# Kernel optimization log

Measured on AMD Instinct MI355X. Metric: run time of the kernel, lower is better.

Reference implementation:

```python
import jax, jax.numpy as jnp
import numpy as np
import math

B, N_NODES, N_EDGES = 2, 20000, 320000
IN_DIM, MODEL_DIM, NUM_HEADS = 128, 128, 8
HEAD_DIM = MODEL_DIM // NUM_HEADS
EPS = 1e-5


def setup_inputs() -> dict:
    key = jax.random.key(0)
    ks = jax.random.split(key, 12)
    s = 0.02
    x = jax.random.normal(ks[0], (B, N_NODES, IN_DIM), dtype=jnp.float32)
    edge_index = jax.random.randint(ks[1], (2, N_EDGES), 0, N_NODES, dtype=jnp.int32)
    return {
        "x": x,
        "proj_w": jax.random.normal(ks[2], (IN_DIM, MODEL_DIM), jnp.float32) * s,
        "wq_w": jax.random.normal(ks[3], (MODEL_DIM, MODEL_DIM), jnp.float32) * s,
        "wq_b": jax.random.normal(ks[4], (MODEL_DIM,), jnp.float32) * s,
        "wk_w": jax.random.normal(ks[5], (MODEL_DIM, MODEL_DIM), jnp.float32) * s,
        "wk_b": jax.random.normal(ks[6], (MODEL_DIM,), jnp.float32) * s,
        "wv_w": jax.random.normal(ks[7], (MODEL_DIM, MODEL_DIM), jnp.float32) * s,
        "wv_b": jax.random.normal(ks[8], (MODEL_DIM,), jnp.float32) * s,
        "ln_g": jnp.ones((MODEL_DIM,), jnp.float32),
        "ln_b": jnp.zeros((MODEL_DIM,), jnp.float32),
        "edge_index": edge_index,
    }


def reference(x, proj_w, wq_w, wq_b, wk_w, wk_b, wv_w, wv_b, ln_g, ln_b, edge_index):
    src, dst = edge_index[0], edge_index[1]
    scale = 1.0 / math.sqrt(HEAD_DIM)

    h = x @ proj_w                      # [B, N, D]  (dropout = identity in eval)
    lifted = h[:, src, :]               # [B, E, D] edge gather
    Q = lifted @ wq_w + wq_b
    K = lifted @ wk_w + wk_b
    V = lifted @ wv_w + wv_b

    alpha = jnp.sum(Q * K, axis=-1) * scale  # [B, E]

    def seg_softmax(a):  # a: [E]
        m = jax.ops.segment_max(a, dst, num_segments=N_NODES)
        m = jnp.where(jnp.isfinite(m), m, 0.0)
        e = jnp.exp(a - m[dst])
        s = jax.ops.segment_sum(e, dst, num_segments=N_NODES)
        return e / s[dst]

    attn = jax.vmap(seg_softmax)(alpha)           # [B, E]
    weighted_V = V * attn[..., None]              # [B, E, D]

    seg_sum = lambda t: jax.ops.segment_sum(t, dst, num_segments=N_NODES)
    agg = jax.vmap(seg_sum)(weighted_V)           # [B, N, D]

    counts = jax.ops.segment_sum(jnp.ones((N_EDGES,), jnp.float32), dst,
                                 num_segments=N_NODES)
    skip = jax.vmap(seg_sum)(lifted) / jnp.maximum(counts, 1.0)[None, :, None]

    out = agg + skip
    mu = jnp.mean(out, axis=-1, keepdims=True)
    var = jnp.var(out, axis=-1, keepdims=True)
    return (out - mu) * jax.lax.rsqrt(var + EPS) * ln_g + ln_b
```

## Files before the change

kernel.cpp:

```cpp
#include <hip/hip_runtime.h>
#include <hip/hip_bf16.h>

#define NNODES 20000
#define NEDGES 320000
#define BATCH  2
#define D      128
#define EPSF   1e-5f
#define QTM    64
#define XS_LD  136
#define MAXDEG 64
#define NROWS  (BATCH * NNODES)

typedef __attribute__((ext_vector_type(8))) short bf16x8;
typedef __attribute__((ext_vector_type(4))) float f32x4;

static __device__ __forceinline__ unsigned short f2bf(float f) {
    __hip_bfloat16 h = __float2bfloat16(f);
    return *reinterpret_cast<unsigned short*>(&h);
}
static __device__ __forceinline__ float bfu(unsigned short u) {
    union { unsigned int i; float f; } cv;
    cv.i = ((unsigned int)u) << 16;
    return cv.f;
}

__global__ __launch_bounds__(256) void prep_kernel(
    const float* __restrict__ Wp, const float* __restrict__ Wq,
    const float* __restrict__ Wk, const float* __restrict__ Wv,
    unsigned short* __restrict__ WF,
    int* __restrict__ cursor)
{
    int bid = blockIdx.x;
    if (bid < 32) {
        int sg = bid * 256 + threadIdx.x;
        int mat = sg >> 11, rem = sg & 2047;
        int f = rem >> 6, l = rem & 63;
        int nt = f >> 2, ks = f & 3;
        int c = l & 15, g = l >> 4;
        const float* W = (mat == 0) ? Wp : (mat == 1) ? Wq : (mat == 2) ? Wk : Wv;
        int n = nt * 16 + c;
        #pragma unroll
        for (int i = 0; i < 8; ++i) {
            int k = ks * 32 + g * 8 + i;
            WF[(size_t)sg * 8 + i] = f2bf(W[k * 128 + n]);
        }
    } else {
        int idx = (bid - 32) * 256 + threadIdx.x;
        if (idx < NNODES) cursor[idx] = 0;
    }
}

__global__ __launch_bounds__(256) void scatter_pad_kernel(
    const int* __restrict__ src, const int* __restrict__ dst,
    int* __restrict__ cursor,
    int* __restrict__ srcs_pad)
{
    int e = blockIdx.x * 256 + threadIdx.x;
    if (e >= NEDGES) return;
    int d = dst[e], s = src[e];
    int slot = atomicAdd(&cursor[d], 1);
    if (slot < MAXDEG) srcs_pad[d * MAXDEG + slot] = s;
}

#define DECL_STAGE_MACROS                                               \
    bf16x8 wreg[8];
#define LOAD_W_REGS(MAT_OFF)                                            \
    _Pragma("unroll")                                                   \
    for (int q = 0; q < 8; ++q)                                         \
        wreg[q] = *(const bf16x8*)(WF + (MAT_OFF) + (q * 256 + t) * 8);
#define WRITE_W_LDS()                                                   \
    _Pragma("unroll")                                                   \
    for (int q = 0; q < 8; ++q)                                         \
        *(bf16x8*)&Wbuf[(q * 256 + t) * 8] = wreg[q];


__global__ __launch_bounds__(256) void hv_kernel(
    const float* __restrict__ x,
    const unsigned short* __restrict__ WF,
    const float* __restrict__ Bv,
    unsigned short* __restrict__ hhv)
{
    __shared__ unsigned short Wbuf[16384];
    __shared__ unsigned short Hs[4][16][XS_LD];
    const int t = threadIdx.x;
    const long row0 = (long)blockIdx.x * QTM;
    const int w = t >> 6, l = t & 63;
    const int g = l >> 4, c = l & 15;
    const int rw = w * 16;
    DECL_STAGE_MACROS

    LOAD_W_REGS(0)

    bf16x8 ax[4];
    {
        const float* xr = x + (row0 + rw + c) * D;
        #pragma unroll
        for (int ks = 0; ks < 4; ++ks) {
            float4 u0 = *(const float4*)(xr + ks * 32 + g * 8);
            float4 u1 = *(const float4*)(xr + ks * 32 + g * 8 + 4);
            bf16x8 f;
            f[0] = (short)f2bf(u0.x); f[1] = (short)f2bf(u0.y);
            f[2] = (short)f2bf(u0.z); f[3] = (short)f2bf(u0.w);
            f[4] = (short)f2bf(u1.x); f[5] = (short)f2bf(u1.y);
            f[6] = (short)f2bf(u1.z); f[7] = (short)f2bf(u1.w);
            ax[ks] = f;
        }
    }

    WRITE_W_LDS();
    __syncthreads();
    LOAD_W_REGS(49152)

    f32x4 hacc[8];
    #pragma unroll
    for (int nt = 0; nt < 8; ++nt) hacc[nt] = f32x4{0.f, 0.f, 0.f, 0.f};
    #pragma unroll
    for (int nt = 0; nt < 8; ++nt)
        #pragma unroll
        for (int ks = 0; ks < 4; ++ks) {
            bf16x8 b = *(const bf16x8*)&Wbuf[((nt * 4 + ks) * 64 + l) * 8];
            hacc[nt] = __builtin_amdgcn_mfma_f32_16x16x32_bf16(ax[ks], b, hacc[nt], 0, 0, 0);
        }
    #pragma unroll
    for (int nt = 0; nt < 8; ++nt)
        #pragma unroll
        for (int i = 0; i < 4; ++i)
            Hs[w][4 * g + i][nt * 16 + c] = f2bf(hacc[nt][i]);

    #pragma unroll
    for (int q = 0; q < 4; ++q) {
        int ch = q * 64 + l;
        int r = ch >> 4, off = (ch & 15) << 3;
        *(bf16x8*)(hhv + (row0 + rw + r) * 256 + off) = *(const bf16x8*)&Hs[w][r][off];
    }
    bf16x8 ah[4];
    #pragma unroll
    for (int ks = 0; ks < 4; ++ks)
        ah[ks] = *(const bf16x8*)&Hs[w][c][ks * 32 + g * 8];

    __syncthreads();
    WRITE_W_LDS();
    __syncthreads();

    #pragma unroll
    for (int nt = 0; nt < 8; ++nt) {
        f32x4 vacc = f32x4{0.f, 0.f, 0.f, 0.f};
        #pragma unroll
        for (int ks = 0; ks < 4; ++ks) {
            bf16x8 b = *(const bf16x8*)&Wbuf[((nt * 4 + ks) * 64 + l) * 8];
            vacc = __builtin_amdgcn_mfma_f32_16x16x32_bf16(ah[ks], b, vacc, 0, 0, 0);
        }
        float bv = Bv[nt * 16 + c];
        #pragma unroll
        for (int i = 0; i < 4; ++i)
            Hs[w][4 * g + i][nt * 16 + c] = f2bf(vacc[i] + bv);
    }
    #pragma unroll
    for (int q = 0; q < 4; ++q) {
        int ch = q * 64 + l;
        int r = ch >> 4, off = (ch & 15) << 3;
        *(bf16x8*)(hhv + (row0 + rw + r) * 256 + 128 + off) = *(const bf16x8*)&Hs[w][r][off];
    }
}

__global__ __launch_bounds__(256) void alpha_kernel(
    const unsigned short* __restrict__ hhv,
    const unsigned short* __restrict__ WF,
    const float* __restrict__ Bq, const float* __restrict__ Bk,
    float* __restrict__ a_out)
{
    __shared__ unsigned short Wbuf[16384];
    const int t = threadIdx.x;
    const long row0 = (long)blockIdx.x * QTM;
    const int w = t >> 6, l = t & 63;
    const int g = l >> 4, c = l & 15;
    const int rw = w * 16;
    DECL_STAGE_MACROS

    LOAD_W_REGS(16384)

    bf16x8 ah[4];
    {
        const unsigned short* hr = hhv + (row0 + rw + c) * 256;
        #pragma unroll
        for (int ks = 0; ks < 4; ++ks)
            ah[ks] = *(const bf16x8*)(hr + ks * 32 + g * 8);
    }

    WRITE_W_LDS();
    __syncthreads();
    LOAD_W_REGS(32768)

    f32x4 qacc[8];
    #pragma unroll
    for (int nt = 0; nt < 8; ++nt) qacc[nt] = f32x4{0.f, 0.f, 0.f, 0.f};
    #pragma unroll
    for (int nt = 0; nt < 8; ++nt)
        #pragma unroll
        for (int ks = 0; ks < 4; ++ks) {
            bf16x8 b = *(const bf16x8*)&Wbuf[((nt * 4 + ks) * 64 + l) * 8];
            qacc[nt] = __builtin_amdgcn_mfma_f32_16x16x32_bf16(ah[ks], b, qacc[nt], 0, 0, 0);
        }
    __syncthreads();
    WRITE_W_LDS();
    __syncthreads();

    float p[4] = {0.f, 0.f, 0.f, 0.f};
    #pragma unroll
    for (int nt = 0; nt < 8; ++nt) {
        f32x4 kacc = f32x4{0.f, 0.f, 0.f, 0.f};
        #pragma unroll
        for (int ks = 0; ks < 4; ++ks) {
            bf16x8 b = *(const bf16x8*)&Wbuf[((nt * 4 + ks) * 64 + l) * 8];
            kacc = __builtin_amdgcn_mfma_f32_16x16x32_bf16(ah[ks], b, kacc, 0, 0, 0);
        }
        float bq = Bq[nt * 16 + c];
        float bk = Bk[nt * 16 + c];
        #pragma unroll
        for (int i = 0; i < 4; ++i)
            p[i] += (qacc[nt][i] + bq) * (kacc[i] + bk);
    }
    #pragma unroll
    for (int off = 1; off < 16; off <<= 1)
        #pragma unroll
        for (int i = 0; i < 4; ++i) p[i] += __shfl_xor(p[i], off, 64);
    if (c == 0)
        #pragma unroll
        for (int i = 0; i < 4; ++i)
            a_out[row0 + rw + 4 * g + i] = p[i] * 0.25f;
}

__global__ __launch_bounds__(256) void agg_kernel(
    const unsigned short* __restrict__ hhv,
    const float* __restrict__ a,
    const int* __restrict__ deg_arr,
    const int* __restrict__ srcs_pad,
    const float* __restrict__ ln_g, const float* __restrict__ ln_b,
    float* __restrict__ out)
{
    const int t = threadIdx.x;
    const int w = t >> 6, l = t & 63;
    const int flat = blockIdx.x * 4 + w;
    const int n = flat % NNODES;
    const int b = flat / NNODES;
    const int bN = b * NNODES;
    const int deg = min(deg_arr[n], MAXDEG);
    const bool valid = l < deg;

    int   sr_l = valid ? srcs_pad[n * MAXDEG + l] : 0;
    float av_l = valid ? a[bN + sr_l] : -1e30f;

    float m = av_l;
    #pragma unroll
    for (int off = 32; off >= 1; off >>= 1) m = fmaxf(m, __shfl_xor(m, off, 64));
    float e_l = valid ? __expf(av_l - m) : 0.f;
    float s = e_l;
    #pragma unroll
    for (int off = 32; off >= 1; off >>= 1) s += __shfl_xor(s, off, 64);
    const float inv_s = (deg > 0) ? 1.f / s : 0.f;
    const float inv_d = 1.f / (float)max(deg, 1);
    const float w_l = e_l * inv_s;

    const int eh   = l >> 5;
    const int half = (l >> 4) & 1;
    const int cq   = l & 15;
    float acc[8] = {0,0,0,0,0,0,0,0};
    const long rowBase = (long)bN * 256 + half * 128 + (cq << 3);

    #define PREP(JJ, OF, MU)  {                                         \
        int sel = ((JJ) << 1) + eh;                                     \
        bool ev = sel < deg;                                            \
        int sc = ev ? sel : 0;                                          \
        int srj = __shfl(sr_l, sc, 64);                                 \
        float wj = __shfl(w_l, sc, 64);                                 \
        MU = half ? (ev ? wj : 0.f) : (ev ? 1.f : 0.f);                 \
        OF = rowBase + (long)srj * 256;  }

    const int iters = (deg + 1) >> 1;
    for (int j0 = 0; j0 < iters; j0 += 4) {
        long oa, ob, oc, od; float ma, mb, mc, md;
        PREP(j0,     oa, ma)
        PREP(j0 + 1, ob, mb)
        PREP(j0 + 2, oc, mc)
        PREP(j0 + 3, od, md)
        bf16x8 da = *(const bf16x8*)(hhv + oa);
        bf16x8 db = *(const bf16x8*)(hhv + ob);
        bf16x8 dc = *(const bf16x8*)(hhv + oc);
        bf16x8 dd = *(const bf16x8*)(hhv + od);
        #pragma unroll
        for (int i = 0; i < 8; ++i) acc[i] += ma * bfu((unsigned short)da[i]);
        #pragma unroll
        for (int i = 0; i < 8; ++i) acc[i] += mb * bfu((unsigned short)db[i]);
        #pragma unroll
        for (int i = 0; i < 8; ++i) acc[i] += mc * bfu((unsigned short)dc[i]);
        #pragma unroll
        for (int i = 0; i < 8; ++i) acc[i] += md * bfu((unsigned short)dd[i]);
    }
    #undef PREP

    float accv[8], sk[8];
    #pragma unroll
    for (int i = 0; i < 8; ++i) {
        float other = __shfl_xor(acc[i], 16, 64);
        accv[i] = half ? acc[i] : other;
        sk[i]   = half ? other  : acc[i];
    }
    #pragma unroll
    for (int i = 0; i < 8; ++i) {
        accv[i] += __shfl_xor(accv[i], 32, 64);
        sk[i]   += __shfl_xor(sk[i],   32, 64);
    }
    float v[8];
    float sum = 0.f, sq = 0.f;
    #pragma unroll
    for (int i = 0; i < 8; ++i) {
        v[i] = accv[i] + sk[i] * inv_d;
        sum += v[i];
        sq  += v[i] * v[i];
    }
    #pragma unroll
    for (int off = 8; off >= 1; off >>= 1) {
        sum += __shfl_xor(sum, off, 64);
        sq  += __shfl_xor(sq,  off, 64);
    }
    float mu   = sum * (1.f / 128.f);
    float var  = sq * (1.f / 128.f) - mu * mu;
    float rstd = rsqrtf(var + EPSF);
    if (l < 16) {
        float4 g0 = *(const float4*)(ln_g + (cq << 3));
        float4 g1 = *(const float4*)(ln_g + (cq << 3) + 4);
        float4 b0 = *(const float4*)(ln_b + (cq << 3));
        float4 b1 = *(const float4*)(ln_b + (cq << 3) + 4);
        float4 o0, o1;
        o0.x = (v[0] - mu) * rstd * g0.x + b0.x;
        o0.y = (v[1] - mu) * rstd * g0.y + b0.y;
        o0.z = (v[2] - mu) * rstd * g0.z + b0.z;
        o0.w = (v[3] - mu) * rstd * g0.w + b0.w;
        o1.x = (v[4] - mu) * rstd * g1.x + b1.x;
        o1.y = (v[5] - mu) * rstd * g1.y + b1.y;
        o1.z = (v[6] - mu) * rstd * g1.z + b1.z;
        o1.w = (v[7] - mu) * rstd * g1.w + b1.w;
        float* op = out + (long)flat * D + (cq << 3);
        *(float4*)op = o0;
        *(float4*)(op + 4) = o1;
    }
}


extern "C" void kernel_launch(void* const* d_in, const int* in_sizes, int n_in,
                              void* d_out, int out_size, void* d_ws, size_t ws_size,
                              hipStream_t stream)
{
    const float* x    = (const float*)d_in[0];
    const float* Wp   = (const float*)d_in[1];
    const float* Wq   = (const float*)d_in[2];
    const float* Bq   = (const float*)d_in[3];
    const float* Wk   = (const float*)d_in[4];
    const float* Bk   = (const float*)d_in[5];
    const float* Wv   = (const float*)d_in[6];
    const float* Bv   = (const float*)d_in[7];
    const float* ln_g = (const float*)d_in[8];
    const float* ln_b = (const float*)d_in[9];
    const int*   ei   = (const int*)d_in[10];
    const int* esrc = ei;
    const int* edst = ei + NEDGES;
    float* out = (float*)d_out;

    char* p = (char*)d_ws;
    auto alloc = [&](size_t bytes) -> char* {
        char* r = p;
        p += (bytes + 255) & ~(size_t)255;
        return r;
    };
    unsigned short* hhv = (unsigned short*)alloc((size_t)NROWS * 256 * 2);
    float* a        = (float*)alloc((size_t)NROWS * 4);
    int* cursor     = (int*)alloc((size_t)NNODES * 4);
    int* srcs_pad   = (int*)alloc((size_t)NNODES * MAXDEG * 4);
    unsigned short* WF = (unsigned short*)alloc((size_t)4 * 128 * 128 * 2);

    prep_kernel<<<111, 256, 0, stream>>>(Wp, Wq, Wk, Wv, WF, cursor);
    scatter_pad_kernel<<<(NEDGES + 255) / 256, 256, 0, stream>>>(esrc, edst, cursor, srcs_pad);
    hv_kernel<<<NROWS / QTM, 256, 0, stream>>>(x, WF, Bv, hhv);
    alpha_kernel<<<NROWS / QTM, 256, 0, stream>>>(hhv, WF, Bq, Bk, a);
    agg_kernel<<<NROWS / 4, 256, 0, stream>>>(hhv, a, cursor, srcs_pad, ln_g, ln_b, out);
}
```

Before: 164.3 us.

## Apply V projection after aggregation instead of per node before gather

Because attention weights sum to one, the V projection and its bias commute with the weighted segment sum. The code therefore aggregates bf16 h rows, both attention-weighted and mean-weighted, and applies Wv in a new final kernel that also does the residual add and LayerNorm. The gather now reads 128-wide h rows instead of 256-wide h|V rows, which halves gather bandwidth. In exchange it adds a kernel launch and an intermediate buffer round-trip, and the final kernel uses uncoalesced scalar loads and stores.

```diff
diff --git a/kernel.cpp b/kernel.cpp
--- a/kernel.cpp
+++ b/kernel.cpp
@@ -73,12 +73,10 @@
     for (int q = 0; q < 8; ++q)                                         \
         *(bf16x8*)&Wbuf[(q * 256 + t) * 8] = wreg[q];
 
-
-__global__ __launch_bounds__(256) void hv_kernel(
+__global__ __launch_bounds__(256) void h_kernel(
     const float* __restrict__ x,
     const unsigned short* __restrict__ WF,
-    const float* __restrict__ Bv,
-    unsigned short* __restrict__ hhv)
+    unsigned short* __restrict__ h_out)
 {
     __shared__ unsigned short Wbuf[16384];
     __shared__ unsigned short Hs[4][16][XS_LD];
@@ -109,7 +107,6 @@
 
     WRITE_W_LDS();
     __syncthreads();
-    LOAD_W_REGS(49152)
 
     f32x4 hacc[8];
     #pragma unroll
@@ -126,45 +123,16 @@
         #pragma unroll
         for (int i = 0; i < 4; ++i)
             Hs[w][4 * g + i][nt * 16 + c] = f2bf(hacc[nt][i]);
-
     #pragma unroll
     for (int q = 0; q < 4; ++q) {
         int ch = q * 64 + l;
         int r = ch >> 4, off = (ch & 15) << 3;
-        *(bf16x8*)(hhv + (row0 + rw + r) * 256 + off) = *(const bf16x8*)&Hs[w][r][off];
-    }
-    bf16x8 ah[4];
-    #pragma unroll
-    for (int ks = 0; ks < 4; ++ks)
-        ah[ks] = *(const bf16x8*)&Hs[w][c][ks * 32 + g * 8];
-
-    __syncthreads();
-    WRITE_W_LDS();
-    __syncthreads();
-
-    #pragma unroll
-    for (int nt = 0; nt < 8; ++nt) {
-        f32x4 vacc = f32x4{0.f, 0.f, 0.f, 0.f};
-        #pragma unroll
-        for (int ks = 0; ks < 4; ++ks) {
-            bf16x8 b = *(const bf16x8*)&Wbuf[((nt * 4 + ks) * 64 + l) * 8];
-            vacc = __builtin_amdgcn_mfma_f32_16x16x32_bf16(ah[ks], b, vacc, 0, 0, 0);
-        }
-        float bv = Bv[nt * 16 + c];
-        #pragma unroll
-        for (int i = 0; i < 4; ++i)
-            Hs[w][4 * g + i][nt * 16 + c] = f2bf(vacc[i] + bv);
-    }
-    #pragma unroll
-    for (int q = 0; q < 4; ++q) {
-        int ch = q * 64 + l;
-        int r = ch >> 4, off = (ch & 15) << 3;
-        *(bf16x8*)(hhv + (row0 + rw + r) * 256 + 128 + off) = *(const bf16x8*)&Hs[w][r][off];
+        *(bf16x8*)(h_out + (row0 + rw + r) * D + off) = *(const bf16x8*)&Hs[w][r][off];
     }
 }
 
 __global__ __launch_bounds__(256) void alpha_kernel(
-    const unsigned short* __restrict__ hhv,
+    const unsigned short* __restrict__ h,
     const unsigned short* __restrict__ WF,
     const float* __restrict__ Bq, const float* __restrict__ Bk,
     float* __restrict__ a_out)
@@ -181,7 +149,7 @@
 
     bf16x8 ah[4];
     {
-        const unsigned short* hr = hhv + (row0 + rw + c) * 256;
+        const unsigned short* hr = h + (row0 + rw + c) * D;
         #pragma unroll
         for (int ks = 0; ks < 4; ++ks)
             ah[ks] = *(const bf16x8*)(hr + ks * 32 + g * 8);
@@ -231,12 +199,12 @@
 }
 
 __global__ __launch_bounds__(256) void agg_kernel(
-    const unsigned short* __restrict__ hhv,
+    const unsigned short* __restrict__ h,
     const float* __restrict__ a,
     const int* __restrict__ deg_arr,
     const int* __restrict__ srcs_pad,
-    const float* __restrict__ ln_g, const float* __restrict__ ln_b,
-    float* __restrict__ out)
+    const float* __restrict__ Bv,
+    unsigned short* __restrict__ HwS)
 {
     const int t = threadIdx.x;
     const int w = t >> 6, l = t & 63;
@@ -261,88 +229,138 @@
     const float inv_d = 1.f / (float)max(deg, 1);
     const float w_l = e_l * inv_s;
 
-    const int eh   = l >> 5;
-    const int half = (l >> 4) & 1;
-    const int cq   = l & 15;
-    float acc[8] = {0,0,0,0,0,0,0,0};
-    const long rowBase = (long)bN * 256 + half * 128 + (cq << 3);
-
-    #define PREP(JJ, OF, MU)  {                                         \
-        int sel = ((JJ) << 1) + eh;                                     \
+    const int eh = l >> 4;
+    const int cq = l & 15;
+    float aw[8] = {0,0,0,0,0,0,0,0};
+    float au[8] = {0,0,0,0,0,0,0,0};
+    const long base = ((long)bN << 7) + (cq << 3);
+
+    #define PREP(JJ, OF, WW, UU)  {                                     \
+        int sel = ((JJ) << 2) + eh;                                     \
         bool ev = sel < deg;                                            \
         int sc = ev ? sel : 0;                                          \
         int srj = __shfl(sr_l, sc, 64);                                 \
         float wj = __shfl(w_l, sc, 64);                                 \
-        MU = half ? (ev ? wj : 0.f) : (ev ? 1.f : 0.f);                 \
-        OF = rowBase + (long)srj * 256;  }
-
-    const int iters = (deg + 1) >> 1;
-    for (int j0 = 0; j0 < iters; j0 += 4) {
-        long oa, ob, oc, od; float ma, mb, mc, md;
-        PREP(j0,     oa, ma)
-        PREP(j0 + 1, ob, mb)
-        PREP(j0 + 2, oc, mc)
-        PREP(j0 + 3, od, md)
-        bf16x8 da = *(const bf16x8*)(hhv + oa);
-        bf16x8 db = *(const bf16x8*)(hhv + ob);
-        bf16x8 dc = *(const bf16x8*)(hhv + oc);
-        bf16x8 dd = *(const bf16x8*)(hhv + od);
-        #pragma unroll
-        for (int i = 0; i < 8; ++i) acc[i] += ma * bfu((unsigned short)da[i]);
-        #pragma unroll
-        for (int i = 0; i < 8; ++i) acc[i] += mb * bfu((unsigned short)db[i]);
-        #pragma unroll
-        for (int i = 0; i < 8; ++i) acc[i] += mc * bfu((unsigned short)dc[i]);
-        #pragma unroll
-        for (int i = 0; i < 8; ++i) acc[i] += md * bfu((unsigned short)dd[i]);
+        WW = ev ? wj : 0.f;                                             \
+        UU = ev ? 1.f : 0.f;                                            \
+        OF = base + ((long)srj << 7);  }
+
+    const int iters = (deg + 3) >> 2;
+    for (int j0 = 0; j0 < iters; j0 += 2) {
+        long oa, ob; float wa, ua, wb, ub;
+        PREP(j0,     oa, wa, ua)
+        PREP(j0 + 1, ob, wb, ub)
+        bf16x8 da = *(const bf16x8*)(h + oa);
+        bf16x8 db = *(const bf16x8*)(h + ob);
+        #pragma unroll
+        for (int i = 0; i < 8; ++i) {
+            float fv = bfu((unsigned short)da[i]);
+            aw[i] += wa * fv;
+            au[i] += ua * fv;
+        }
+        #pragma unroll
+        for (int i = 0; i < 8; ++i) {
+            float fv = bfu((unsigned short)db[i]);
+            aw[i] += wb * fv;
+            au[i] += ub * fv;
+        }
     }
     #undef PREP
 
-    float accv[8], sk[8];
     #pragma unroll
     for (int i = 0; i < 8; ++i) {
-        float other = __shfl_xor(acc[i], 16, 64);
-        accv[i] = half ? acc[i] : other;
-        sk[i]   = half ? other  : acc[i];
-    }
-    #pragma unroll
-    for (int i = 0; i < 8; ++i) {
-        accv[i] += __shfl_xor(accv[i], 32, 64);
-        sk[i]   += __shfl_xor(sk[i],   32, 64);
-    }
-    float v[8];
-    float sum = 0.f, sq = 0.f;
-    #pragma unroll
-    for (int i = 0; i < 8; ++i) {
-        v[i] = accv[i] + sk[i] * inv_d;
-        sum += v[i];
-        sq  += v[i] * v[i];
-    }
-    #pragma unroll
-    for (int off = 8; off >= 1; off >>= 1) {
-        sum += __shfl_xor(sum, off, 64);
-        sq  += __shfl_xor(sq,  off, 64);
-    }
-    float mu   = sum * (1.f / 128.f);
-    float var  = sq * (1.f / 128.f) - mu * mu;
-    float rstd = rsqrtf(var + EPSF);
+        aw[i] += __shfl_xor(aw[i], 16, 64);
+        au[i] += __shfl_xor(au[i], 16, 64);
+        aw[i] += __shfl_xor(aw[i], 32, 64);
+        au[i] += __shfl_xor(au[i], 32, 64);
+    }
     if (l < 16) {
-        float4 g0 = *(const float4*)(ln_g + (cq << 3));
-        float4 g1 = *(const float4*)(ln_g + (cq << 3) + 4);
-        float4 b0 = *(const float4*)(ln_b + (cq << 3));
-        float4 b1 = *(const float4*)(ln_b + (cq << 3) + 4);
-        float4 o0, o1;
-        o0.x = (v[0] - mu) * rstd * g0.x + b0.x;
-        o0.y = (v[1] - mu) * rstd * g0.y + b0.y;
-        o0.z = (v[2] - mu) * rstd * g0.z + b0.z;
-        o0.w = (v[3] - mu) * rstd * g0.w + b0.w;
-        o1.x = (v[4] - mu) * rstd * g1.x + b1.x;
-        o1.y = (v[5] - mu) * rstd * g1.y + b1.y;
-        o1.z = (v[6] - mu) * rstd * g1.z + b1.z;
-        o1.w = (v[7] - mu) * rstd * g1.w + b1.w;
-        float* op = out + (long)flat * D + (cq << 3);
-        *(float4*)op = o0;
-        *(float4*)(op + 4) = o1;
+        const float bvm = (deg > 0) ? 1.f : 0.f;
+        bf16x8 w8, s8;
+        #pragma unroll
+        for (int i = 0; i < 8; ++i) {
+            w8[i] = (short)f2bf(aw[i]);
+            s8[i] = (short)f2bf(au[i] * inv_d + bvm * Bv[(cq << 3) + i]);
+        }
+        unsigned short* op = HwS + (long)flat * 256 + (cq << 3);
+        *(bf16x8*)op = w8;
+        *(bf16x8*)(op + 128) = s8;
+    }
+}
+
+__global__ __launch_bounds__(256) void final_kernel(
+    const unsigned short* __restrict__ HwS,
+    const unsigned short* __restrict__ WF,
+    const float* __restrict__ ln_g, const float* __restrict__ ln_b,
+    float* __restrict__ out)
+{
+    __shared__ unsigned short Wbuf[16384];
+    const int t = threadIdx.x;
+    const long row0 = (long)blockIdx.x * QTM;
+    const int w = t >> 6, l = t & 63;
+    const int g = l >> 4, c = l & 15;
+    const int rw = w * 16;
+    DECL_STAGE_MACROS
+
+    LOAD_W_REGS(49152)
+
+    bf16x8 ah[4];
+    {
+        const unsigned short* hr = HwS + (row0 + rw + c) * 256;
+        #pragma unroll
+        for (int ks = 0; ks < 4; ++ks)
+            ah[ks] = *(const bf16x8*)(hr + ks * 32 + g * 8);
+    }
+
+    WRITE_W_LDS();
+    __syncthreads();
+
+    float val[8][4];
+    #pragma unroll
+    for (int nt = 0; nt < 8; ++nt) {
+        f32x4 vacc = f32x4{0.f, 0.f, 0.f, 0.f};
+        #pragma unroll
+        for (int ks = 0; ks < 4; ++ks) {
+            bf16x8 b = *(const bf16x8*)&Wbuf[((nt * 4 + ks) * 64 + l) * 8];
+            vacc = __builtin_amdgcn_mfma_f32_16x16x32_bf16(ah[ks], b, vacc, 0, 0, 0);
+        }
+        #pragma unroll
+        for (int i = 0; i < 4; ++i) {
+            long R = row0 + rw + 4 * g + i;
+            val[nt][i] = vacc[i] + bfu(HwS[R * 256 + 128 + nt * 16 + c]);
+        }
+    }
+    float sum[4] = {0,0,0,0}, sq[4] = {0,0,0,0};
+    #pragma unroll
+    for (int nt = 0; nt < 8; ++nt)
+        #pragma unroll
+        for (int i = 0; i < 4; ++i) {
+            sum[i] += val[nt][i];
+            sq[i]  += val[nt][i] * val[nt][i];
+        }
+    #pragma unroll
+    for (int off = 8; off >= 1; off >>= 1)
+        #pragma unroll
+        for (int i = 0; i < 4; ++i) {
+            sum[i] += __shfl_xor(sum[i], off, 64);
+            sq[i]  += __shfl_xor(sq[i],  off, 64);
+        }
+    float mu[4], rstd[4];
+    #pragma unroll
+    for (int i = 0; i < 4; ++i) {
+        mu[i] = sum[i] * (1.f / 128.f);
+        float var = sq[i] * (1.f / 128.f) - mu[i] * mu[i];
+        rstd[i] = rsqrtf(var + EPSF);
+    }
+    #pragma unroll
+    for (int nt = 0; nt < 8; ++nt) {
+        float gg = ln_g[nt * 16 + c];
+        float bb = ln_b[nt * 16 + c];
+        #pragma unroll
+        for (int i = 0; i < 4; ++i) {
+            long R = row0 + rw + 4 * g + i;
+            out[R * D + nt * 16 + c] = (val[nt][i] - mu[i]) * rstd[i] * gg + bb;
+        }
     }
 }
 
@@ -372,7 +390,8 @@
         p += (bytes + 255) & ~(size_t)255;
         return r;
     };
-    unsigned short* hhv = (unsigned short*)alloc((size_t)NROWS * 256 * 2);
+    unsigned short* h   = (unsigned short*)alloc((size_t)NROWS * D * 2);
+    unsigned short* HwS = (unsigned short*)alloc((size_t)NROWS * 256 * 2);
     float* a        = (float*)alloc((size_t)NROWS * 4);
     int* cursor     = (int*)alloc((size_t)NNODES * 4);
     int* srcs_pad   = (int*)alloc((size_t)NNODES * MAXDEG * 4);
@@ -380,7 +399,8 @@
 
     prep_kernel<<<111, 256, 0, stream>>>(Wp, Wq, Wk, Wv, WF, cursor);
     scatter_pad_kernel<<<(NEDGES + 255) / 256, 256, 0, stream>>>(esrc, edst, cursor, srcs_pad);
-    hv_kernel<<<NROWS / QTM, 256, 0, stream>>>(x, WF, Bv, hhv);
-    alpha_kernel<<<NROWS / QTM, 256, 0, stream>>>(hhv, WF, Bq, Bk, a);
-    agg_kernel<<<NROWS / 4, 256, 0, stream>>>(hhv, a, cursor, srcs_pad, ln_g, ln_b, out);
-}
+    h_kernel<<<NROWS / QTM, 256, 0, stream>>>(x, WF, h);
+    alpha_kernel<<<NROWS / QTM, 256, 0, stream>>>(h, WF, Bq, Bk, a);
+    agg_kernel<<<NROWS / 4, 256, 0, stream>>>(h, a, cursor, srcs_pad, Bv, HwS);
+    final_kernel<<<NROWS / QTM, 256, 0, stream>>>(HwS, WF, ln_g, ln_b, out);
+}
```

Result: faster. 159.6 us (-2.9%).
